# Performance work log

Measured on AMD Instinct MI355X. Metric: run time of the kernel, lower is better.

Reference implementation:

```python
import jax, jax.numpy as jnp
import numpy as np

EPS = 1e-6

def setup_inputs() -> dict:
    key = jax.random.key(0)
    k1, k2, k3 = jax.random.split(key, 3)
    D = 1024
    return {
        "x": jax.random.normal(k1, (2, 2048, D), dtype=jnp.float32),
        "w_norm": jnp.ones((D,), dtype=jnp.float32),
        "w_qkv": jax.random.normal(k2, (3 * D, D), dtype=jnp.float32) * (1.0 / np.sqrt(D)),
        "w_out": jax.random.normal(k3, (D, D), dtype=jnp.float32) * (1.0 / np.sqrt(D)),
        "window_size": 128,
        "n_heads": 16,
    }

def reference(x, w_norm, w_qkv, w_out, window_size, n_heads):
    B, L, D = x.shape
    H = n_heads
    dh = D // H
    skip = x
    # RMSNorm
    rms = jnp.sqrt(jnp.mean(x * x, axis=-1, keepdims=True) + EPS)
    xn = w_norm * (x / rms)
    # QKV projection (torch Linear: y = x @ W.T)
    qkv = xn @ w_qkv.T  # [B, L, 3D]
    q, k, v = jnp.split(qkv, 3, axis=-1)
    q = q.reshape(B, L, H, dh).transpose(0, 2, 1, 3)  # [B,H,L,dh]
    k = k.reshape(B, L, H, dh).transpose(0, 2, 1, 3)
    v = v.reshape(B, L, H, dh).transpose(0, 2, 1, 3)
    scores = jnp.einsum("bhid,bhjd->bhij", q, k) / np.sqrt(dh)  # [B,H,L,L]
    # Symmetric window: token i attends to j in [i - w//2, i + w//2]
    idx = jnp.arange(L)
    half = window_size // 2
    band = jnp.abs(idx[:, None] - idx[None, :]) <= half  # [L, L]
    scores = jnp.where(band, scores, -jnp.inf)
    attn = jax.nn.softmax(scores, axis=-1)  # zeros outside band, matches torch loop
    out = jnp.einsum("bhij,bhjd->bhid", attn, v)  # [B,H,L,dh]
    out = out.transpose(0, 2, 1, 3).reshape(B, L, D)
    out = out @ w_out.T
    return out + skip
```

## Files before the change

kernel.cpp:

```cpp
#include <hip/hip_runtime.h>
#include <hip/hip_bf16.h>
#include <cstdint>

typedef float f32x4 __attribute__((ext_vector_type(4)));
typedef short s16x8 __attribute__((ext_vector_type(8)));
typedef short s16x4 __attribute__((ext_vector_type(4)));

constexpr int B_ = 2, L_ = 2048, D_ = 1024, H_ = 16, DH = 64, HALF = 64;
constexpr int M_ROWS = B_ * L_;
constexpr int QKV_N = 3 * D_;

__device__ __forceinline__ void gload16(const void* g, void* l) {
    __builtin_amdgcn_global_load_lds(
        (const __attribute__((address_space(1))) unsigned int*)g,
        (__attribute__((address_space(3))) unsigned int*)l, 16, 0, 0);
}

__global__ void rmsnorm_kernel(const float* __restrict__ x, const float* __restrict__ wn,
                               __hip_bfloat16* __restrict__ xn) {
    int row = blockIdx.x;
    int t = threadIdx.x;
    const float4* xr = reinterpret_cast<const float4*>(x + (size_t)row * D_);
    float4 v = xr[t];
    float ss = v.x * v.x + v.y * v.y + v.z * v.z + v.w * v.w;
#pragma unroll
    for (int off = 32; off; off >>= 1) ss += __shfl_xor(ss, off);
    __shared__ float red[4];
    if ((t & 63) == 0) red[t >> 6] = ss;
    __syncthreads();
    float tot = red[0] + red[1] + red[2] + red[3];
    float rinv = rsqrtf(tot * (1.0f / D_) + 1e-6f);
    const float4* wr = reinterpret_cast<const float4*>(wn);
    float4 w = wr[t];
    __hip_bfloat16* o = xn + (size_t)row * D_ + t * 4;
    o[0] = __float2bfloat16(v.x * rinv * w.x);
    o[1] = __float2bfloat16(v.y * rinv * w.y);
    o[2] = __float2bfloat16(v.z * rinv * w.z);
    o[3] = __float2bfloat16(v.w * rinv * w.w);
}

__global__ void cvt_weights_kernel(const float* __restrict__ wq, const float* __restrict__ wo,
                                   __hip_bfloat16* __restrict__ oq, __hip_bfloat16* __restrict__ oo) {
    constexpr int NQ4 = QKV_N * D_ / 4;
    int i = blockIdx.x * blockDim.x + threadIdx.x;
    const float* src; __hip_bfloat16* dst; int j;
    if (i < NQ4) { src = wq; dst = oq; j = i; }
    else         { src = wo; dst = oo; j = i - NQ4; }
    float4 v = reinterpret_cast<const float4*>(src)[j];
    __hip_bfloat16* o = dst + (size_t)j * 4;
    o[0] = __float2bfloat16(v.x);
    o[1] = __float2bfloat16(v.y);
    o[2] = __float2bfloat16(v.z);
    o[3] = __float2bfloat16(v.w);
}

template <int EPI>
__global__ __launch_bounds__(256, 2) void gemm_pipe_kernel(const __hip_bfloat16* __restrict__ A,
                                                           const __hip_bfloat16* __restrict__ Bt,
                                                           __hip_bfloat16* __restrict__ Cbf,
                                                           __hip_bfloat16* __restrict__ vT,
                                                           float* __restrict__ Cf,
                                                           const float* __restrict__ resid,
                                                           int M, int N, int K) {
    constexpr int BM = 128, BN = 128;
    constexpr int BUF = (BM + BN) * 128;
    __shared__ __align__(16) char smem[2 * BUF];

    const int tid = threadIdx.x;
    const int lane = tid & 63;
    const int wid = tid >> 6;

    int nwg = gridDim.x * gridDim.y;
    int lin = blockIdx.y * gridDim.x + blockIdx.x;
    int cpx = nwg >> 3;
    int swz = (lin & 7) * cpx + (lin >> 3);
    int bx = swz % gridDim.x;
    int by = swz / gridDim.x;

    const int rowBase = by * BM;
    const int colBase = bx * BN;
    const int NTILES = K >> 6;

    const int srow = tid >> 3;
    const int colSw = ((tid & 7) ^ (srow & 7)) << 3;
    const __hip_bfloat16* aG = A + (size_t)(rowBase + srow) * K + colSw;
    const __hip_bfloat16* bG = Bt + (size_t)(colBase + srow) * K + colSw;
    const int dstW = wid << 10;

    const int wm = wid >> 1, wn = wid & 1;
    const int l15 = lane & 15, hi = lane >> 4;
    const int s7 = l15 & 7;
    const int rA = wm * 64 + l15;
    const int rB = wn * 64 + l15;

    f32x4 acc[4][4];
#pragma unroll
    for (int m = 0; m < 4; ++m)
#pragma unroll
        for (int n = 0; n < 4; ++n) acc[m][n] = (f32x4){0.f, 0.f, 0.f, 0.f};

#pragma unroll
    for (int i = 0; i < 4; ++i) {
        gload16(aG + (size_t)(i * 32) * K, smem + i * 4096 + dstW);
        gload16(bG + (size_t)(i * 32) * K, smem + BM * 128 + i * 4096 + dstW);
    }

    for (int kt = 0; kt < NTILES; ++kt) {
        const int bf = kt & 1;
        __builtin_amdgcn_s_barrier();
        if (kt + 1 < NTILES) {
            char* base = smem + (bf ^ 1) * BUF;
            const __hip_bfloat16* as = aG + (size_t)(kt + 1) * 64;
            const __hip_bfloat16* bs = bG + (size_t)(kt + 1) * 64;
#pragma unroll
            for (int i = 0; i < 4; ++i) {
                gload16(as + (size_t)(i * 32) * K, base + i * 4096 + dstW);
                gload16(bs + (size_t)(i * 32) * K, base + BM * 128 + i * 4096 + dstW);
            }
            asm volatile("s_waitcnt vmcnt(8)" ::: "memory");
        } else {
            asm volatile("s_waitcnt vmcnt(0)" ::: "memory");
        }

        const char* ab = smem + bf * BUF;
        const char* bb = ab + BM * 128;
        s16x8 af[4][2], bfr[4][2];
#pragma unroll
        for (int mf = 0; mf < 4; ++mf)
#pragma unroll
            for (int kk = 0; kk < 2; ++kk)
                af[mf][kk] = *(const s16x8*)(ab + (rA + mf * 16) * 128 + (((kk * 4 + hi) ^ s7) << 4));
#pragma unroll
        for (int nf = 0; nf < 4; ++nf)
#pragma unroll
            for (int kk = 0; kk < 2; ++kk)
                bfr[nf][kk] = *(const s16x8*)(bb + (rB + nf * 16) * 128 + (((kk * 4 + hi) ^ s7) << 4));

        __builtin_amdgcn_s_setprio(1);
#pragma unroll
        for (int kk = 0; kk < 2; ++kk)
#pragma unroll
            for (int mf = 0; mf < 4; ++mf)
#pragma unroll
                for (int nf = 0; nf < 4; ++nf)
                    acc[mf][nf] = __builtin_amdgcn_mfma_f32_16x16x32_bf16(af[mf][kk], bfr[nf][kk],
                                                                          acc[mf][nf], 0, 0, 0);
        __builtin_amdgcn_s_setprio(0);
    }

#pragma unroll
    for (int mf = 0; mf < 4; ++mf) {
#pragma unroll
        for (int nf = 0; nf < 4; ++nf) {
            int col = colBase + wn * 64 + nf * 16 + l15;
            int row0 = rowBase + wm * 64 + mf * 16 + 4 * hi;
            if (EPI == 0) {
                if (col < 2 * D_) {
#pragma unroll
                    for (int r = 0; r < 4; ++r)
                        Cbf[(size_t)(row0 + r) * N + col] = __float2bfloat16(acc[mf][nf][r]);
                } else {
                    int h = (col - 2 * D_) >> 6;
                    int dim = (col - 2 * D_) & 63;
                    int bb2 = row0 >> 11, i0 = row0 & (L_ - 1);
                    s16x4 pk;
#pragma unroll
                    for (int r = 0; r < 4; ++r) {
                        __hip_bfloat16 t = __float2bfloat16(acc[mf][nf][r]);
                        pk[r] = *reinterpret_cast<short*>(&t);
                    }
                    *(s16x4*)(vT + ((size_t)(bb2 * H_ + h) * DH + dim) * L_ + i0) = pk;
                }
            } else {
#pragma unroll
                for (int r = 0; r < 4; ++r)
                    Cf[(size_t)(row0 + r) * N + col] = acc[mf][nf][r] + resid[(size_t)(row0 + r) * N + col];
            }
        }
    }
}

__global__ __launch_bounds__(128) void attn_mfma_kernel(const __hip_bfloat16* __restrict__ qkv,
                                                        const __hip_bfloat16* __restrict__ vT,
                                                        __hip_bfloat16* __restrict__ attn) {
    __shared__ __align__(16) char smem[57344];
    constexpr int VOFF = 24576;
    int tid = threadIdx.x;
    int lane = tid & 63, w = tid >> 6;
    int tq = blockIdx.x, h = blockIdx.y, b = blockIdx.z;
    int q0 = tq * 64;
    int jg0 = q0 - HALF;
    const __hip_bfloat16* qkvb = qkv + (size_t)(b * L_) * QKV_N;
    const __hip_bfloat16* vTg = vT + (size_t)(b * H_ + h) * DH * L_;

#pragma unroll
    for (int it = 0; it < 12; ++it) {
        int ob = (it * 2 + w) << 10;
        int o = ob + lane * 16;
        int row = o >> 7;
        int c = ((o >> 4) & 7) ^ (row & 7);
        int jg = jg0 + row;
        int jc = jg < 0 ? 0 : (jg > L_ - 1 ? L_ - 1 : jg);
        gload16(qkvb + (size_t)jc * QKV_N + D_ + h * DH + c * 8, smem + ob);
    }
#pragma unroll
    for (int it = 0; it < 16; ++it) {
        int ob = (it * 2 + w) << 10;
        int o = ob + lane * 16;
        int d = o >> 9;
        int c = ((o >> 4) & 31) ^ (d & 7);
        int kb = jg0 + c * 8;
        int kc = kb < 0 ? 0 : (kb > L_ - 8 ? L_ - 8 : kb);
        gload16(vTg + (size_t)d * L_ + kc, smem + VOFF + ob);
    }
    __syncthreads();

    int l15 = lane & 15, hi = lane >> 4;

    s16x8 aq[2][2];
#pragma unroll
    for (int m = 0; m < 2; ++m)
#pragma unroll
        for (int kk = 0; kk < 2; ++kk)
            aq[m][kk] = *(const s16x8*)(qkvb + (size_t)(q0 + 32 * w + 16 * m + l15) * QKV_N
                                        + h * DH + kk * 32 + hi * 8);

    f32x4 sc[2][10];
#pragma unroll
    for (int m = 0; m < 2; ++m)
#pragma unroll
        for (int kt = 0; kt < 10; ++kt) sc[m][kt] = (f32x4){0.f, 0.f, 0.f, 0.f};

#pragma unroll
    for (int kt = 0; kt < 10; ++kt) {
        int jl = 32 * w + 16 * kt + l15;
        s16x8 bk0 = *(const s16x8*)(smem + jl * 128 + ((hi ^ (jl & 7)) * 16));
        s16x8 bk1 = *(const s16x8*)(smem + jl * 128 + (((4 + hi) ^ (jl & 7)) * 16));
#pragma unroll
        for (int m = 0; m < 2; ++m) {
            sc[m][kt] = __builtin_amdgcn_mfma_f32_16x16x32_bf16(aq[m][0], bk0, sc[m][kt], 0, 0, 0);
            sc[m][kt] = __builtin_amdgcn_mfma_f32_16x16x32_bf16(aq[m][1], bk1, sc[m][kt], 0, 0, 0);
        }
    }

#pragma unroll
    for (int m = 0; m < 2; ++m) {
#pragma unroll
        for (int r = 0; r < 4; ++r) {
            int iloc = 32 * w + 16 * m + 4 * hi + r;
            float mx = -1e30f;
#pragma unroll
            for (int kt = 0; kt < 10; ++kt) {
                int jl = 32 * w + 16 * kt + l15;
                int jg = jg0 + jl;
                bool ok = (jl >= iloc) && (jl <= iloc + 2 * HALF) && (jg >= 0) && (jg < L_);
                float s = ok ? sc[m][kt][r] * 0.125f : -1e30f;
                sc[m][kt][r] = s;
                mx = fmaxf(mx, s);
            }
            mx = fmaxf(mx, __shfl_xor(mx, 1));
            mx = fmaxf(mx, __shfl_xor(mx, 2));
            mx = fmaxf(mx, __shfl_xor(mx, 4));
            mx = fmaxf(mx, __shfl_xor(mx, 8));
            float sum = 0.f;
#pragma unroll
            for (int kt = 0; kt < 10; ++kt) {
                float p = __expf(sc[m][kt][r] - mx);
                sc[m][kt][r] = p;
                sum += p;
            }
            sum += __shfl_xor(sum, 1);
            sum += __shfl_xor(sum, 2);
            sum += __shfl_xor(sum, 4);
            sum += __shfl_xor(sum, 8);
            float inv = 1.0f / sum;
#pragma unroll
            for (int kt = 0; kt < 10; ++kt) sc[m][kt][r] *= inv;
        }
    }

    __syncthreads();

    {
        __hip_bfloat16* Pw = (__hip_bfloat16*)(smem + w * 10752);
#pragma unroll
        for (int m = 0; m < 2; ++m)
#pragma unroll
            for (int kt = 0; kt < 10; ++kt)
#pragma unroll
                for (int r = 0; r < 4; ++r)
                    Pw[(16 * m + 4 * hi + r) * 168 + 16 * kt + l15] = __float2bfloat16(sc[m][kt][r]);
    }
    __syncthreads();

    f32x4 o[2][4];
#pragma unroll
    for (int m = 0; m < 2; ++m)
#pragma unroll
        for (int nt = 0; nt < 4; ++nt) o[m][nt] = (f32x4){0.f, 0.f, 0.f, 0.f};

#pragma unroll
    for (int kst = 0; kst < 5; ++kst) {
        s16x8 ap[2];
#pragma unroll
        for (int m = 0; m < 2; ++m)
            ap[m] = *(const s16x8*)(smem + w * 10752 + (16 * m + l15) * 336 + (32 * kst + 8 * hi) * 2);
#pragma unroll
        for (int nt = 0; nt < 4; ++nt) {
            int d = 16 * nt + l15;
            int c = 4 * w + 4 * kst + hi;
            s16x8 bv = *(const s16x8*)(smem + VOFF + d * 512 + ((c ^ (d & 7)) << 4));
#pragma unroll
            for (int m = 0; m < 2; ++m)
                o[m][nt] = __builtin_amdgcn_mfma_f32_16x16x32_bf16(ap[m], bv, o[m][nt], 0, 0, 0);
        }
    }

#pragma unroll
    for (int m = 0; m < 2; ++m)
#pragma unroll
        for (int nt = 0; nt < 4; ++nt)
#pragma unroll
            for (int r = 0; r < 4; ++r) {
                int rowg = q0 + 32 * w + 16 * m + 4 * hi + r;
                attn[(size_t)(b * L_ + rowg) * D_ + h * DH + 16 * nt + l15] =
                    __float2bfloat16(o[m][nt][r]);
            }
}

extern "C" void kernel_launch(void* const* d_in, const int* in_sizes, int n_in,
                              void* d_out, int out_size, void* d_ws, size_t ws_size,
                              hipStream_t stream) {
    const float* x      = (const float*)d_in[0];
    const float* w_norm = (const float*)d_in[1];
    const float* w_qkv  = (const float*)d_in[2];
    const float* w_out  = (const float*)d_in[3];

    char* ws = (char*)d_ws;
    __hip_bfloat16* xn   = (__hip_bfloat16*)(ws);
    __hip_bfloat16* wq   = (__hip_bfloat16*)(ws + (8u  << 20));
    __hip_bfloat16* wo   = (__hip_bfloat16*)(ws + (14u << 20));
    __hip_bfloat16* qkv  = (__hip_bfloat16*)(ws + (16u << 20));
    __hip_bfloat16* attn = (__hip_bfloat16*)(ws + (40u << 20));
    __hip_bfloat16* vT   = (__hip_bfloat16*)(ws + (48u << 20));
    float* out = (float*)d_out;

    {
        int n4 = (QKV_N * D_ + D_ * D_) / 4;
        cvt_weights_kernel<<<n4 / 256, 256, 0, stream>>>(w_qkv, w_out, wq, wo);
    }

    rmsnorm_kernel<<<M_ROWS, 256, 0, stream>>>(x, w_norm, xn);

    gemm_pipe_kernel<0><<<dim3(QKV_N / 128, M_ROWS / 128), 256, 0, stream>>>(
        xn, wq, qkv, vT, nullptr, nullptr, M_ROWS, QKV_N, D_);

    attn_mfma_kernel<<<dim3(L_ / 64, H_, B_), 128, 0, stream>>>(qkv, vT, attn);

    gemm_pipe_kernel<1><<<dim3(D_ / 128, M_ROWS / 128), 256, 0, stream>>>(
        attn, wo, nullptr, nullptr, out, x, M_ROWS, D_, D_);
}
```

Baseline: 93.34 us.

## Rework rmsnorm, GEMM pipeline sync, vT epilogue, and attention V staging

RMSNorm now runs one row per wavefront with no shared-memory reduction, and both RMSNorm and weight conversion pack their bf16 outputs into vector stores. The GEMM is templated on BN: the output projection uses BN=64 so it launches more workgroups, and the barrier is moved after the wait, with a trailing barrier and LDS wait added. The V-transpose epilogue now stages through LDS and writes contiguous 16-byte chunks instead of scattered 8-byte stores. The attention kernel loads Q before issuing the async loads, stages only 384 bytes of V per dimension to cut LDS use, and overlaps the V loads with the start of compute using a partial vmcnt wait. The extra barriers and the smaller tile for the output GEMM could add sync overhead or reduce data reuse.

```diff
diff --git a/kernel.cpp b/kernel.cpp
--- a/kernel.cpp
+++ b/kernel.cpp
@@ -16,27 +16,41 @@
         (__attribute__((address_space(3))) unsigned int*)l, 16, 0, 0);
 }
 
-__global__ void rmsnorm_kernel(const float* __restrict__ x, const float* __restrict__ wn,
-                               __hip_bfloat16* __restrict__ xn) {
-    int row = blockIdx.x;
-    int t = threadIdx.x;
+__device__ __forceinline__ void cfence() {
+    __builtin_amdgcn_sched_barrier(0);
+    asm volatile("" ::: "memory");
+}
+
+__global__ __launch_bounds__(256) void rmsnorm_kernel(const float* __restrict__ x,
+                                                      const float* __restrict__ wn,
+                                                      __hip_bfloat16* __restrict__ xn) {
+    int w = threadIdx.x >> 6, lane = threadIdx.x & 63;
+    int row = blockIdx.x * 4 + w;
     const float4* xr = reinterpret_cast<const float4*>(x + (size_t)row * D_);
-    float4 v = xr[t];
-    float ss = v.x * v.x + v.y * v.y + v.z * v.z + v.w * v.w;
+    const float4* wr = reinterpret_cast<const float4*>(wn);
+    float4 v[4];
+    float ss = 0.f;
+#pragma unroll
+    for (int c = 0; c < 4; ++c) {
+        v[c] = xr[c * 64 + lane];
+        ss += v[c].x * v[c].x + v[c].y * v[c].y + v[c].z * v[c].z + v[c].w * v[c].w;
+    }
 #pragma unroll
     for (int off = 32; off; off >>= 1) ss += __shfl_xor(ss, off);
-    __shared__ float red[4];
-    if ((t & 63) == 0) red[t >> 6] = ss;
-    __syncthreads();
-    float tot = red[0] + red[1] + red[2] + red[3];
-    float rinv = rsqrtf(tot * (1.0f / D_) + 1e-6f);
-    const float4* wr = reinterpret_cast<const float4*>(wn);
-    float4 w = wr[t];
-    __hip_bfloat16* o = xn + (size_t)row * D_ + t * 4;
-    o[0] = __float2bfloat16(v.x * rinv * w.x);
-    o[1] = __float2bfloat16(v.y * rinv * w.y);
-    o[2] = __float2bfloat16(v.z * rinv * w.z);
-    o[3] = __float2bfloat16(v.w * rinv * w.w);
+    float rinv = rsqrtf(ss * (1.0f / D_) + 1e-6f);
+#pragma unroll
+    for (int c = 0; c < 4; ++c) {
+        float4 wv = wr[c * 64 + lane];
+        s16x4 pk;
+        float vals[4] = {v[c].x * rinv * wv.x, v[c].y * rinv * wv.y,
+                         v[c].z * rinv * wv.z, v[c].w * rinv * wv.w};
+#pragma unroll
+        for (int e = 0; e < 4; ++e) {
+            __hip_bfloat16 t = __float2bfloat16(vals[e]);
+            pk[e] = *reinterpret_cast<short*>(&t);
+        }
+        *(s16x4*)(xn + (size_t)row * D_ + (c * 64 + lane) * 4) = pk;
+    }
 }
 
 __global__ void cvt_weights_kernel(const float* __restrict__ wq, const float* __restrict__ wo,
@@ -47,14 +61,17 @@
     if (i < NQ4) { src = wq; dst = oq; j = i; }
     else         { src = wo; dst = oo; j = i - NQ4; }
     float4 v = reinterpret_cast<const float4*>(src)[j];
-    __hip_bfloat16* o = dst + (size_t)j * 4;
-    o[0] = __float2bfloat16(v.x);
-    o[1] = __float2bfloat16(v.y);
-    o[2] = __float2bfloat16(v.z);
-    o[3] = __float2bfloat16(v.w);
-}
-
-template <int EPI>
+    s16x4 pk;
+    float vals[4] = {v.x, v.y, v.z, v.w};
+#pragma unroll
+    for (int e = 0; e < 4; ++e) {
+        __hip_bfloat16 t = __float2bfloat16(vals[e]);
+        pk[e] = *reinterpret_cast<short*>(&t);
+    }
+    *(s16x4*)(dst + (size_t)j * 4) = pk;
+}
+
+template <int EPI, int BN>
 __global__ __launch_bounds__(256, 2) void gemm_pipe_kernel(const __hip_bfloat16* __restrict__ A,
                                                            const __hip_bfloat16* __restrict__ Bt,
                                                            __hip_bfloat16* __restrict__ Cbf,
@@ -62,8 +79,12 @@
                                                            float* __restrict__ Cf,
                                                            const float* __restrict__ resid,
                                                            int M, int N, int K) {
-    constexpr int BM = 128, BN = 128;
-    constexpr int BUF = (BM + BN) * 128;
+    constexpr int BM = 128;
+    constexpr int NFR = BN / 32;
+    constexpr int ABYTES = BM * 128;
+    constexpr int BBYTES = BN * 128;
+    constexpr int BUF = ABYTES + BBYTES;
+    constexpr int AISS = BM / 32, BISS = BN / 32, NISS = AISS + BISS;
     __shared__ __align__(16) char smem[2 * BUF];
 
     const int tid = threadIdx.x;
@@ -91,47 +112,49 @@
     const int l15 = lane & 15, hi = lane >> 4;
     const int s7 = l15 & 7;
     const int rA = wm * 64 + l15;
-    const int rB = wn * 64 + l15;
-
-    f32x4 acc[4][4];
+    const int rB = wn * (BN / 2) + l15;
+
+    f32x4 acc[4][NFR];
 #pragma unroll
     for (int m = 0; m < 4; ++m)
 #pragma unroll
-        for (int n = 0; n < 4; ++n) acc[m][n] = (f32x4){0.f, 0.f, 0.f, 0.f};
-
-#pragma unroll
-    for (int i = 0; i < 4; ++i) {
-        gload16(aG + (size_t)(i * 32) * K, smem + i * 4096 + dstW);
-        gload16(bG + (size_t)(i * 32) * K, smem + BM * 128 + i * 4096 + dstW);
-    }
+        for (int n = 0; n < NFR; ++n) acc[m][n] = (f32x4){0.f, 0.f, 0.f, 0.f};
+
+#pragma unroll
+    for (int i = 0; i < AISS; ++i) gload16(aG + (size_t)(i * 32) * K, smem + i * 4096 + dstW);
+#pragma unroll
+    for (int i = 0; i < BISS; ++i) gload16(bG + (size_t)(i * 32) * K, smem + ABYTES + i * 4096 + dstW);
 
     for (int kt = 0; kt < NTILES; ++kt) {
         const int bf = kt & 1;
-        __builtin_amdgcn_s_barrier();
         if (kt + 1 < NTILES) {
             char* base = smem + (bf ^ 1) * BUF;
             const __hip_bfloat16* as = aG + (size_t)(kt + 1) * 64;
             const __hip_bfloat16* bs = bG + (size_t)(kt + 1) * 64;
 #pragma unroll
-            for (int i = 0; i < 4; ++i) {
-                gload16(as + (size_t)(i * 32) * K, base + i * 4096 + dstW);
-                gload16(bs + (size_t)(i * 32) * K, base + BM * 128 + i * 4096 + dstW);
-            }
-            asm volatile("s_waitcnt vmcnt(8)" ::: "memory");
+            for (int i = 0; i < AISS; ++i) gload16(as + (size_t)(i * 32) * K, base + i * 4096 + dstW);
+#pragma unroll
+            for (int i = 0; i < BISS; ++i) gload16(bs + (size_t)(i * 32) * K, base + ABYTES + i * 4096 + dstW);
+            if constexpr (NISS == 8)
+                asm volatile("s_waitcnt vmcnt(8)" ::: "memory");
+            else
+                asm volatile("s_waitcnt vmcnt(6)" ::: "memory");
         } else {
             asm volatile("s_waitcnt vmcnt(0)" ::: "memory");
         }
+        __builtin_amdgcn_s_barrier();
+        cfence();
 
         const char* ab = smem + bf * BUF;
-        const char* bb = ab + BM * 128;
-        s16x8 af[4][2], bfr[4][2];
+        const char* bb = ab + ABYTES;
+        s16x8 af[4][2], bfr[NFR][2];
 #pragma unroll
         for (int mf = 0; mf < 4; ++mf)
 #pragma unroll
             for (int kk = 0; kk < 2; ++kk)
                 af[mf][kk] = *(const s16x8*)(ab + (rA + mf * 16) * 128 + (((kk * 4 + hi) ^ s7) << 4));
 #pragma unroll
-        for (int nf = 0; nf < 4; ++nf)
+        for (int nf = 0; nf < NFR; ++nf)
 #pragma unroll
             for (int kk = 0; kk < 2; ++kk)
                 bfr[nf][kk] = *(const s16x8*)(bb + (rB + nf * 16) * 128 + (((kk * 4 + hi) ^ s7) << 4));
@@ -142,48 +165,72 @@
 #pragma unroll
             for (int mf = 0; mf < 4; ++mf)
 #pragma unroll
-                for (int nf = 0; nf < 4; ++nf)
+                for (int nf = 0; nf < NFR; ++nf)
                     acc[mf][nf] = __builtin_amdgcn_mfma_f32_16x16x32_bf16(af[mf][kk], bfr[nf][kk],
                                                                           acc[mf][nf], 0, 0, 0);
         __builtin_amdgcn_s_setprio(0);
-    }
-
-#pragma unroll
-    for (int mf = 0; mf < 4; ++mf) {
-#pragma unroll
-        for (int nf = 0; nf < 4; ++nf) {
-            int col = colBase + wn * 64 + nf * 16 + l15;
-            int row0 = rowBase + wm * 64 + mf * 16 + 4 * hi;
-            if (EPI == 0) {
-                if (col < 2 * D_) {
+
+        asm volatile("s_waitcnt lgkmcnt(0)" ::: "memory");
+        __builtin_amdgcn_s_barrier();
+        cfence();
+    }
+
+    if constexpr (EPI == 0) {
+        if (colBase < 2 * D_) {
+#pragma unroll
+            for (int mf = 0; mf < 4; ++mf)
+#pragma unroll
+                for (int nf = 0; nf < NFR; ++nf) {
+                    int col = colBase + wn * (BN / 2) + nf * 16 + l15;
+                    int row0 = rowBase + wm * 64 + mf * 16 + 4 * hi;
 #pragma unroll
                     for (int r = 0; r < 4; ++r)
                         Cbf[(size_t)(row0 + r) * N + col] = __float2bfloat16(acc[mf][nf][r]);
-                } else {
-                    int h = (col - 2 * D_) >> 6;
-                    int dim = (col - 2 * D_) & 63;
-                    int bb2 = row0 >> 11, i0 = row0 & (L_ - 1);
-                    s16x4 pk;
+                }
+        } else {
+            char* Ct = smem;
+#pragma unroll
+            for (int mf = 0; mf < 4; ++mf)
+#pragma unroll
+                for (int nf = 0; nf < NFR; ++nf) {
+                    int cl = wn * (BN / 2) + nf * 16 + l15;
 #pragma unroll
                     for (int r = 0; r < 4; ++r) {
+                        int rl = wm * 64 + mf * 16 + 4 * hi + r;
                         __hip_bfloat16 t = __float2bfloat16(acc[mf][nf][r]);
-                        pk[r] = *reinterpret_cast<short*>(&t);
+                        *(short*)(Ct + cl * 272 + rl * 2) = *reinterpret_cast<short*>(&t);
                     }
-                    *(s16x4*)(vT + ((size_t)(bb2 * H_ + h) * DH + dim) * L_ + i0) = pk;
                 }
-            } else {
+            __syncthreads();
+            int cl = tid >> 1, half = tid & 1;
+            int gcol = colBase + cl - 2 * D_;
+            int hh = gcol >> 6, dd = gcol & 63;
+            int bb2 = rowBase >> 11, i0 = rowBase & (L_ - 1);
+            __hip_bfloat16* dstp = vT + ((size_t)(bb2 * H_ + hh) * DH + dd) * L_ + i0 + half * 64;
+#pragma unroll
+            for (int ch = 0; ch < 8; ++ch) {
+                s16x8 vv = *(const s16x8*)(Ct + cl * 272 + half * 128 + ch * 16);
+                *(s16x8*)(dstp + ch * 8) = vv;
+            }
+        }
+    } else {
+#pragma unroll
+        for (int mf = 0; mf < 4; ++mf)
+#pragma unroll
+            for (int nf = 0; nf < NFR; ++nf) {
+                int col = colBase + wn * (BN / 2) + nf * 16 + l15;
+                int row0 = rowBase + wm * 64 + mf * 16 + 4 * hi;
 #pragma unroll
                 for (int r = 0; r < 4; ++r)
                     Cf[(size_t)(row0 + r) * N + col] = acc[mf][nf][r] + resid[(size_t)(row0 + r) * N + col];
             }
-        }
     }
 }
 
 __global__ __launch_bounds__(128) void attn_mfma_kernel(const __hip_bfloat16* __restrict__ qkv,
                                                         const __hip_bfloat16* __restrict__ vT,
                                                         __hip_bfloat16* __restrict__ attn) {
-    __shared__ __align__(16) char smem[57344];
+    __shared__ __align__(16) char smem[49152];
     constexpr int VOFF = 24576;
     int tid = threadIdx.x;
     int lane = tid & 63, w = tid >> 6;
@@ -193,6 +240,16 @@
     const __hip_bfloat16* qkvb = qkv + (size_t)(b * L_) * QKV_N;
     const __hip_bfloat16* vTg = vT + (size_t)(b * H_ + h) * DH * L_;
 
+    int l15 = lane & 15, hi = lane >> 4;
+
+    s16x8 aq[2][2];
+#pragma unroll
+    for (int m = 0; m < 2; ++m)
+#pragma unroll
+        for (int kk = 0; kk < 2; ++kk)
+            aq[m][kk] = *(const s16x8*)(qkvb + (size_t)(q0 + 32 * w + 16 * m + l15) * QKV_N
+                                        + h * DH + kk * 32 + hi * 8);
+
 #pragma unroll
     for (int it = 0; it < 12; ++it) {
         int ob = (it * 2 + w) << 10;
@@ -204,26 +261,19 @@
         gload16(qkvb + (size_t)jc * QKV_N + D_ + h * DH + c * 8, smem + ob);
     }
 #pragma unroll
-    for (int it = 0; it < 16; ++it) {
+    for (int it = 0; it < 12; ++it) {
         int ob = (it * 2 + w) << 10;
         int o = ob + lane * 16;
-        int d = o >> 9;
-        int c = ((o >> 4) & 31) ^ (d & 7);
+        int d = o / 384;
+        int rem = o - d * 384;
+        int c = (rem >> 4) ^ (d & 7);
         int kb = jg0 + c * 8;
         int kc = kb < 0 ? 0 : (kb > L_ - 8 ? L_ - 8 : kb);
         gload16(vTg + (size_t)d * L_ + kc, smem + VOFF + ob);
     }
-    __syncthreads();
-
-    int l15 = lane & 15, hi = lane >> 4;
-
-    s16x8 aq[2][2];
-#pragma unroll
-    for (int m = 0; m < 2; ++m)
-#pragma unroll
-        for (int kk = 0; kk < 2; ++kk)
-            aq[m][kk] = *(const s16x8*)(qkvb + (size_t)(q0 + 32 * w + 16 * m + l15) * QKV_N
-                                        + h * DH + kk * 32 + hi * 8);
+    asm volatile("s_waitcnt vmcnt(12)" ::: "memory");
+    __builtin_amdgcn_s_barrier();
+    cfence();
 
     f32x4 sc[2][10];
 #pragma unroll
@@ -309,7 +359,7 @@
         for (int nt = 0; nt < 4; ++nt) {
             int d = 16 * nt + l15;
             int c = 4 * w + 4 * kst + hi;
-            s16x8 bv = *(const s16x8*)(smem + VOFF + d * 512 + ((c ^ (d & 7)) << 4));
+            s16x8 bv = *(const s16x8*)(smem + VOFF + d * 384 + ((c ^ (d & 7)) << 4));
 #pragma unroll
             for (int m = 0; m < 2; ++m)
                 o[m][nt] = __builtin_amdgcn_mfma_f32_16x16x32_bf16(ap[m], bv, o[m][nt], 0, 0, 0);
@@ -350,13 +400,13 @@
         cvt_weights_kernel<<<n4 / 256, 256, 0, stream>>>(w_qkv, w_out, wq, wo);
     }
 
-    rmsnorm_kernel<<<M_ROWS, 256, 0, stream>>>(x, w_norm, xn);
-
-    gemm_pipe_kernel<0><<<dim3(QKV_N / 128, M_ROWS / 128), 256, 0, stream>>>(
+    rmsnorm_kernel<<<M_ROWS / 4, 256, 0, stream>>>(x, w_norm, xn);
+
+    gemm_pipe_kernel<0, 128><<<dim3(QKV_N / 128, M_ROWS / 128), 256, 0, stream>>>(
         xn, wq, qkv, vT, nullptr, nullptr, M_ROWS, QKV_N, D_);
 
     attn_mfma_kernel<<<dim3(L_ / 64, H_, B_), 128, 0, stream>>>(qkv, vT, attn);
 
-    gemm_pipe_kernel<1><<<dim3(D_ / 128, M_ROWS / 128), 256, 0, stream>>>(
+    gemm_pipe_kernel<1, 64><<<dim3(D_ / 64, M_ROWS / 128), 256, 0, stream>>>(
         attn, wo, nullptr, nullptr, out, x, M_ROWS, D_, D_);
 }
```

Result: no change. 92.35 us (-1.1%).
